# Kernel optimization log

Measured on AMD Instinct MI355X. Metric: run time of the kernel, lower is better.

## Reference

```python
import jax, jax.numpy as jnp
import numpy as np

D_MODEL = 1024
NHEAD = 16
D_K = D_MODEL // NHEAD  # 64
B, L = 2, 2048


def _apply_rotary(x, cos, sin):
    # x: (B, H, L, d_k); cos/sin: (B, L, d_k//2)
    d_half = x.shape[-1] // 2
    x1, x2 = x[..., :d_half], x[..., d_half:]
    c = cos[:, None, :, :]
    s = sin[:, None, :, :]
    return jnp.concatenate([x1 * c - x2 * s, x1 * s + x2 * c], axis=-1)


def setup_inputs() -> dict:
    key = jax.random.key(0)
    ks = jax.random.split(key, 7)
    x = jax.random.normal(ks[0], (B, L, D_MODEL), dtype=jnp.float32)
    rope_cos = jax.random.uniform(ks[1], (B, L, D_K // 2), dtype=jnp.float32)
    rope_sin = jax.random.uniform(ks[2], (B, L, D_K // 2), dtype=jnp.float32)
    # Linear params (PyTorch layout: weight (out, in), y = x @ W.T + b)
    lim_qkv = 1.0 / np.sqrt(D_MODEL)
    W_qkv = jax.random.uniform(ks[3], (3 * D_MODEL, D_MODEL), dtype=jnp.float32, minval=-lim_qkv, maxval=lim_qkv)
    b_qkv = jax.random.uniform(ks[4], (3 * D_MODEL,), dtype=jnp.float32, minval=-lim_qkv, maxval=lim_qkv)
    W_out = jax.random.uniform(ks[5], (D_MODEL, D_MODEL), dtype=jnp.float32, minval=-lim_qkv, maxval=lim_qkv)
    b_out = jax.random.uniform(ks[6], (D_MODEL,), dtype=jnp.float32, minval=-lim_qkv, maxval=lim_qkv)
    return {"x": x, "rope_cos": rope_cos, "rope_sin": rope_sin,
            "W_qkv": W_qkv, "b_qkv": b_qkv, "W_out": W_out, "b_out": b_out}


def reference(x, rope_cos, rope_sin, W_qkv, b_qkv, W_out, b_out):
    Bx, Lx, D = x.shape
    scale = D_K ** -0.5
    qkv = x @ W_qkv.T + b_qkv                     # (B, L, 3D)
    qkv = qkv.reshape(Bx, Lx, 3, NHEAD, D_K)
    q = jnp.transpose(qkv[:, :, 0], (0, 2, 1, 3))  # (B, H, L, d_k)
    k = jnp.transpose(qkv[:, :, 1], (0, 2, 1, 3))
    v = jnp.transpose(qkv[:, :, 2], (0, 2, 1, 3))
    q = _apply_rotary(q, rope_cos, rope_sin)
    k = _apply_rotary(k, rope_cos, rope_sin)
    attn = jnp.einsum("bhqd,bhkd->bhqk", q, k) * scale  # (B, H, L, L)
    attn = jax.nn.softmax(attn, axis=-1)
    out = jnp.einsum("bhqk,bhkd->bhqd", attn, v)          # (B, H, L, d_k)
    out = jnp.transpose(out, (0, 2, 1, 3)).reshape(Bx, Lx, D)
    return out @ W_out.T + b_out
```

## Files before the change

kernel.cpp:

```cpp
#include <hip/hip_runtime.h>
#include <hip/hip_bf16.h>
#include <stdint.h>


typedef __attribute__((ext_vector_type(8)))  short bf16x8;
typedef __attribute__((ext_vector_type(4)))  float f32x4;
typedef __attribute__((ext_vector_type(16))) float f32x16;
typedef __attribute__((ext_vector_type(4)))  short short4v;
typedef __attribute__((ext_vector_type(4)))  unsigned int u32x4;

#define DEV static __device__ __forceinline__

DEV short f2bf(float f) {
  uint32_t u = __builtin_bit_cast(uint32_t, f);
  u += 0x7FFFu + ((u >> 16) & 1u);
  return (short)(u >> 16);
}
DEV float bf2f(short s) {
  return __builtin_bit_cast(float, ((uint32_t)(uint16_t)s) << 16);
}
DEV uint32_t pkbf(float a, float b) {
  __hip_bfloat162 h = __float22bfloat162_rn(make_float2(a, b));
  uint32_t u;
  __builtin_memcpy(&u, &h, 4);
  return u;
}
DEV void pl32swap(uint32_t &dst, uint32_t &src) {
  asm volatile("v_permlane32_swap_b32 %0, %1" : "+v"(dst), "+v"(src));
}

#define AS1 __attribute__((address_space(1)))
#define AS3 __attribute__((address_space(3)))
#define GLOAD_LDS16(gp, lp) \
  __builtin_amdgcn_global_load_lds((const AS1 void*)(gp), (AS3 void*)(lp), 16, 0, 0)

__global__ void k_cvt_all(const float* __restrict__ x, const float* __restrict__ wq,
                          const float* __restrict__ wo,
                          short* __restrict__ xb, short* __restrict__ wqb,
                          short* __restrict__ wob) {
  int bid = blockIdx.x;
  const float* in;
  short* out;
  int i;
  if (bid < 4096)      { in = x;  out = xb;  i = bid * 256 + threadIdx.x; }
  else if (bid < 7168) { in = wq; out = wqb; i = (bid - 4096) * 256 + threadIdx.x; }
  else                 { in = wo; out = wob; i = (bid - 7168) * 256 + threadIdx.x; }
  float4 v = reinterpret_cast<const float4*>(in)[i];
  short4v o = { f2bf(v.x), f2bf(v.y), f2bf(v.z), f2bf(v.w) };
  reinterpret_cast<short4v*>(out)[i] = o;
}

DEV void gemm_stage(const short* Ag, const short* Bg, int K_,
                    short* AsD, short* BsD, int tid) {
  #pragma unroll
  for (int p = 0; p < 4; ++p) {
    int f = p * 256 + tid;
    int row = f >> 3;
    int sch = (f & 7) ^ (row & 7);
    GLOAD_LDS16(Ag + (size_t)row * K_ + sch * 8, AsD + f * 8);
    GLOAD_LDS16(Bg + (size_t)row * K_ + sch * 8, BsD + f * 8);
  }
}

#define GEMM_BODY(A_, Bt_, K_)                                              \
  __shared__ short Lds[4 * 128 * 64];    \
  const int tid = threadIdx.x;                                              \
  const int lane = tid & 63;                                                \
  const int wid  = tid >> 6;                                                \
  const int lq = lane & 15, lg = lane >> 4;                                 \
  const int wr = wid >> 1, wc = wid & 1;                                    \
  int lin_ = blockIdx.y * gridDim.x + blockIdx.x;                           \
  const int q_ = (gridDim.x * gridDim.y) >> 3;                              \
  lin_ = (lin_ & 7) * q_ + (lin_ >> 3);                                     \
  const int m0 = (lin_ / gridDim.x) * 128;                                  \
  const int n0 = (lin_ % gridDim.x) * 128;                                  \
  f32x4 acc[4][4];                                                          \
  _Pragma("unroll")                                                         \
  for (int i = 0; i < 4; ++i)                                               \
    _Pragma("unroll")                                                       \
    for (int j = 0; j < 4; ++j) acc[i][j] = (f32x4){0.f, 0.f, 0.f, 0.f};    \
  const int KT = (K_) >> 6;                                                 \
  gemm_stage((A_) + (size_t)m0 * (K_), (Bt_) + (size_t)n0 * (K_), (K_),     \
             Lds, Lds + 8192, tid);                                         \
  __syncthreads();                                                          \
  int gbuf = 0;                                                             \
  for (int kt = 0; kt < KT; ++kt) {                                         \
    if (kt + 1 < KT)                                                        \
      gemm_stage((A_)  + (size_t)m0 * (K_) + (kt + 1) * 64,                 \
                 (Bt_) + (size_t)n0 * (K_) + (kt + 1) * 64, (K_),           \
                 Lds + (gbuf ^ 1) * 16384,                                  \
                 Lds + (gbuf ^ 1) * 16384 + 8192, tid);                     \
    const short* As = Lds + gbuf * 16384;                                   \
    const short* Bs = As + 8192;                                            \
    _Pragma("unroll")                                                       \
    for (int kk = 0; kk < 2; ++kk) {                                        \
      bf16x8 af[4], bfr[4];                                                 \
      _Pragma("unroll")                                                     \
      for (int i = 0; i < 4; ++i)                                           \
        af[i]  = *reinterpret_cast<const bf16x8*>(                          \
            &As[(wr*64 + i*16 + lq) * 64 + (((kk*4 + lg) ^ (lq & 7)) * 8)]);\
      _Pragma("unroll")                                                     \
      for (int j = 0; j < 4; ++j)                                           \
        bfr[j] = *reinterpret_cast<const bf16x8*>(                          \
            &Bs[(wc*64 + j*16 + lq) * 64 + (((kk*4 + lg) ^ (lq & 7)) * 8)]);\
      _Pragma("unroll")                                                     \
      for (int i = 0; i < 4; ++i)                                           \
        _Pragma("unroll")                                                   \
        for (int j = 0; j < 4; ++j)                                         \
          acc[i][j] = __builtin_amdgcn_mfma_f32_16x16x32_bf16(              \
              af[i], bfr[j], acc[i][j], 0, 0, 0);                           \
    }                                                                       \
    __syncthreads();                                                        \
    gbuf ^= 1;                                                              \
  }

__global__ __launch_bounds__(256) void k_gemm_qkv(
    const short* __restrict__ A, const short* __restrict__ Bt,
    const float* __restrict__ bias,
    const float* __restrict__ cosb, const float* __restrict__ sinb,
    short* __restrict__ Qb, short* __restrict__ Kb, short* __restrict__ Vt)
{
  GEMM_BODY(A, Bt, 1024)

  short* Ep = Lds + wid * 4096;
  const int cglob = n0 + wc * 64;
  if (cglob < 2048) {
    const bool isq = (cglob < 1024);
    const float QS = isq ? 0.125f * 1.4426950408889634f : 1.0f;
    short* dst = isq ? Qb : Kb;
    const int h = (cglob & 1023) >> 6;
    const float b0 = bias[cglob + lq],      b2 = bias[cglob + 32 + lq];
    const float b1 = bias[cglob + 16 + lq], b3 = bias[cglob + 48 + lq];
    #pragma unroll
    for (int i = 0; i < 4; ++i) {
      #pragma unroll
      for (int r = 0; r < 4; ++r) {
        int lloc = i*16 + lg*4 + r;
        int rg = m0 + wr*64 + lloc;
        float c0 = cosb[(size_t)rg * 32 + lq];
        float s0 = sinb[(size_t)rg * 32 + lq];
        float c1 = cosb[(size_t)rg * 32 + 16 + lq];
        float s1 = sinb[(size_t)rg * 32 + 16 + lq];
        float x1 = acc[i][0][r] + b0, x2 = acc[i][2][r] + b2;
        Ep[lloc*64 + lq]      = f2bf((x1 * c0 - x2 * s0) * QS);
        Ep[lloc*64 + 32 + lq] = f2bf((x1 * s0 + x2 * c0) * QS);
        float y1 = acc[i][1][r] + b1, y2 = acc[i][3][r] + b3;
        Ep[lloc*64 + 16 + lq] = f2bf((y1 * c1 - y2 * s1) * QS);
        Ep[lloc*64 + 48 + lq] = f2bf((y1 * s1 + y2 * c1) * QS);
      }
    }
    #pragma unroll
    for (int p = 0; p < 8; ++p) {
      int f = p * 64 + lane;
      int lloc = f >> 3, d0 = (f & 7) * 8;
      int rg = m0 + wr*64 + lloc;
      int bi = rg >> 11, ll = rg & 2047;
      bf16x8 v = *reinterpret_cast<const bf16x8*>(&Ep[lloc*64 + d0]);
      *reinterpret_cast<bf16x8*>(
          &dst[((size_t)(bi * 16 + h) * 2048 + ll) * 64 + d0]) = v;
    }
  } else {
    const int h = (cglob - 2048) >> 6;
    #pragma unroll
    for (int i = 0; i < 4; ++i) {
      int lloc = i*16 + lg*4;
      #pragma unroll
      for (int j = 0; j < 4; ++j) {
        int d = j * 16 + lq;
        float bv = bias[cglob + d];
        short4v pk4 = { f2bf(acc[i][j][0] + bv), f2bf(acc[i][j][1] + bv),
                        f2bf(acc[i][j][2] + bv), f2bf(acc[i][j][3] + bv) };
        *reinterpret_cast<short4v*>(
            &Ep[d*64 + (lloc ^ ((d & 7) << 3))]) = pk4;
      }
    }
    #pragma unroll
    for (int p = 0; p < 8; ++p) {
      int f = p * 64 + lane;
      int d = f >> 3, lc = (f & 7) * 8;
      bf16x8 v = *reinterpret_cast<const bf16x8*>(&Ep[d*64 + lc]);
      int lreal = lc ^ ((d & 7) << 3);
      int rg = m0 + wr*64 + lreal;
      int bi = rg >> 11, ll = rg & 2047;
      *reinterpret_cast<bf16x8*>(
          &Vt[((size_t)(bi * 16 + h) * 64 + d) * 2048 + ll]) = v;
    }
  }
}

__global__ __launch_bounds__(256) void k_gemm_out(
    const short* __restrict__ A, const short* __restrict__ Bt,
    const float* __restrict__ bias, float* __restrict__ C)
{
  GEMM_BODY(A, Bt, 1024)
  const int N = 1024;
  #pragma unroll
  for (int i = 0; i < 4; ++i) {
    int rbase = m0 + wr*64 + i*16 + lg*4;
    #pragma unroll
    for (int j = 0; j < 4; ++j) {
      int col = n0 + wc*64 + j*16 + lq;
      float bv = bias[col];
      #pragma unroll
      for (int r = 0; r < 4; ++r)
        C[(size_t)(rbase + r) * N + col] = acc[i][j][r] + bv;
    }
  }
}

__global__ __launch_bounds__(256, 4) void k_attn(
    const short* __restrict__ Q, const short* __restrict__ Kb,
    const short* __restrict__ Vt,
    short* __restrict__ P0, short* __restrict__ P1,
    float* __restrict__ L0, float* __restrict__ L1)
{
  __shared__ short Ks[2][64 * 64];
  __shared__ short Vs[2][64 * 64];
  const int tid = threadIdx.x;
  const int lane = tid & 63;
  const int wid  = tid >> 6;
  const int Lq = lane & 31;
  const int h  = lane >> 5;
  const int bh = blockIdx.y;
  const int q0 = blockIdx.x * 128 + wid * 32;
  const int b = bh >> 4, hh = bh & 15;
  const int t0 = blockIdx.z * 16;
  short* Pp = blockIdx.z ? P1 : P0;
  float* Lp = blockIdx.z ? L1 : L0;

  const short* Qp = Q  + ((size_t)bh * 2048 + q0 + Lq) * 64;
  const short* Kp = Kb + (size_t)bh * 2048 * 64;
  const short* Vp = Vt + (size_t)bh * 64 * 2048;

  #define STAGE_KV(c, t) do {                                              \
    const short* Kg_ = Kp + (size_t)(t) * 64 * 64;                         \
    const short* Vg_ = Vp + (size_t)(t) * 64;                              \
    _Pragma("unroll")                                                      \
    for (int p_ = 0; p_ < 2; ++p_) {                                       \
      int f_ = p_ * 256 + tid;                                             \
      int row_ = f_ >> 3;                                                  \
      int sch_ = (f_ & 7) ^ (row_ & 7);                                    \
      GLOAD_LDS16(Kg_ + row_ * 64 + sch_ * 8,            &Ks[c][f_ * 8]);  \
      GLOAD_LDS16(Vg_ + (size_t)row_ * 2048 + sch_ * 8,  &Vs[c][f_ * 8]);  \
    }                                                                      \
  } while (0)

  bf16x8 qf[4];
  #pragma unroll
  for (int ks = 0; ks < 4; ++ks)
    qf[ks] = *reinterpret_cast<const bf16x8*>(Qp + ks * 16 + h * 8);

  f32x16 o[2];
  #pragma unroll
  for (int nd = 0; nd < 2; ++nd)
    #pragma unroll
    for (int r = 0; r < 16; ++r) o[nd][r] = 0.f;
  float la0 = 0.f, la1 = 0.f;

  STAGE_KV(0, t0);
  asm volatile("s_waitcnt vmcnt(0)" ::: "memory");
  __syncthreads();

  for (int kk2 = 0; kk2 < 16; ++kk2) {
    const int cur = kk2 & 1;
    if (kk2 < 15) STAGE_KV(cur ^ 1, t0 + kk2 + 1);

    #pragma unroll
    for (int mb = 0; mb < 2; ++mb) {
      f32x16 sm;
      #pragma unroll
      for (int r = 0; r < 16; ++r) sm[r] = 0.f;
      #pragma unroll
      for (int ks = 0; ks < 4; ++ks) {
        bf16x8 kf = *reinterpret_cast<const bf16x8*>(
            &Ks[cur][(mb*32 + Lq) * 64 + (((ks*2 + h) ^ (Lq & 7)) * 8)]);
        sm = __builtin_amdgcn_mfma_f32_32x32x16_bf16(kf, qf[ks], sm, 0, 0, 0);
      }
      #pragma unroll
      for (int half = 0; half < 2; ++half) {
        float e0 = __builtin_amdgcn_exp2f(sm[8*half + 0]);
        float e1 = __builtin_amdgcn_exp2f(sm[8*half + 1]);
        float e2 = __builtin_amdgcn_exp2f(sm[8*half + 2]);
        float e3 = __builtin_amdgcn_exp2f(sm[8*half + 3]);
        float e4 = __builtin_amdgcn_exp2f(sm[8*half + 4]);
        float e5 = __builtin_amdgcn_exp2f(sm[8*half + 5]);
        float e6 = __builtin_amdgcn_exp2f(sm[8*half + 6]);
        float e7 = __builtin_amdgcn_exp2f(sm[8*half + 7]);
        la0 += (e0 + e1) + (e4 + e5);
        la1 += (e2 + e3) + (e6 + e7);
        uint32_t w0 = pkbf(e0, e1), w1 = pkbf(e2, e3);
        uint32_t w2 = pkbf(e4, e5), w3 = pkbf(e6, e7);
        pl32swap(w0, w2);
        pl32swap(w1, w3);
        u32x4 paw = { w0, w1, w2, w3 };
        bf16x8 pa = __builtin_bit_cast(bf16x8, paw);
        const int ksl = mb * 2 + half;
        #pragma unroll
        for (int nd = 0; nd < 2; ++nd) {
          bf16x8 vf = *reinterpret_cast<const bf16x8*>(
              &Vs[cur][(nd*32 + Lq) * 64 + (((ksl*2 + h) ^ (Lq & 7)) * 8)]);
          o[nd] = __builtin_amdgcn_mfma_f32_32x32x16_bf16(pa, vf, o[nd], 0, 0, 0);
        }
      }
    }
    asm volatile("s_waitcnt vmcnt(0)" ::: "memory");
    __syncthreads();
  }

  float l_part = la0 + la1;
  l_part += __shfl_xor(l_part, 32, 64);
  if (h == 0) Lp[((size_t)bh << 11) + q0 + Lq] = l_part;
  #pragma unroll
  for (int r = 0; r < 16; ++r) {
    int qrow = (r & 3) + 8 * (r >> 2) + 4 * h;
    size_t rowb = ((size_t)b * 2048 + q0 + qrow) * 1024 + hh * 64;
    Pp[rowb + Lq]      = f2bf(o[0][r]);
    Pp[rowb + 32 + Lq] = f2bf(o[1][r]);
  }
  #undef STAGE_KV
}

__global__ void k_merge(const short* __restrict__ P0, const short* __restrict__ P1,
                        const float* __restrict__ L0, const float* __restrict__ L1,
                        short* __restrict__ AO)
{
  int idx = blockIdx.x * 256 + threadIdx.x;
  int rg = idx >> 7;
  int c0 = (idx & 127) * 8;
  int bh = ((rg >> 11) << 4) + (c0 >> 6);
  size_t lix = ((size_t)bh << 11) + (rg & 2047);
  float inv = 1.f / (L0[lix] + L1[lix]);
  size_t off = (size_t)rg * 1024 + c0;
  bf16x8 a = *reinterpret_cast<const bf16x8*>(&P0[off]);
  bf16x8 bv = *reinterpret_cast<const bf16x8*>(&P1[off]);
  bf16x8 r;
  #pragma unroll
  for (int j = 0; j < 8; ++j)
    r[j] = f2bf((bf2f(a[j]) + bf2f(bv[j])) * inv);
  *reinterpret_cast<bf16x8*>(&AO[off]) = r;
}

extern "C" void kernel_launch(void* const* d_in, const int* in_sizes, int n_in,
                              void* d_out, int out_size, void* d_ws, size_t ws_size,
                              hipStream_t stream) {
  (void)in_sizes; (void)n_in; (void)out_size; (void)ws_size;
  const float* x    = (const float*)d_in[0];
  const float* rc   = (const float*)d_in[1];
  const float* rs   = (const float*)d_in[2];
  const float* Wqkv = (const float*)d_in[3];
  const float* bqkv = (const float*)d_in[4];
  const float* Wout = (const float*)d_in[5];
  const float* bout = (const float*)d_in[6];
  float* out = (float*)d_out;

  char* ws = (char*)d_ws;
  short* xb  = (short*)(ws);
  short* wqb = (short*)(ws + 8388608);
  short* wob = (short*)(ws + 14680064);
  short* Qb  = (short*)(ws + 16777216);
  short* Kb  = (short*)(ws + 25165824);
  short* Vt  = (short*)(ws + 33554432);
  short* P0  = (short*)(ws + 41943040);
  short* P1  = (short*)(ws + 50331648);
  float* L0  = (float*)(ws + 58720256);
  float* L1  = (float*)(ws + 58982400);

  k_cvt_all<<<8192, 256, 0, stream>>>(x, Wqkv, Wout, xb, wqb, wob);
  k_gemm_qkv<<<dim3(24, 32), 256, 0, stream>>>(xb, wqb, bqkv, rc, rs, Qb, Kb, Vt);
  k_attn<<<dim3(16, 32, 2), 256, 0, stream>>>(Qb, Kb, Vt, P0, P1, L0, L1);
  k_merge<<<2048, 256, 0, stream>>>(P0, P1, L0, L1, P0);
  k_gemm_out<<<dim3(8, 32), 256, 0, stream>>>(P0, wob, bout, out);
}
```

Measured before the change: 115.3 us.

## Use 4-stage LDS pipeline with K=32 slices and vmcnt waits in GEMMs

Replaces the double-buffered 64-wide K tiles with a four-stage ring of 32-wide K slices in the same LDS footprint. Three slices are prefetched ahead, and partial s_waitcnt vmcnt waits with a single barrier per step replace the full __syncthreads pair, so global-to-LDS loads overlap deeper with MFMA work. It changes the XOR swizzle for the narrower rows. The cost is more loop iterations with fewer MFMAs each and hand-tuned wait counts that must match the issued load count.

After: 115.1 us. About the same (-0.2%).

```diff
diff --git a/kernel.cpp b/kernel.cpp
--- a/kernel.cpp
+++ b/kernel.cpp
@@ -50,20 +50,8 @@
   reinterpret_cast<short4v*>(out)[i] = o;
 }
 
-DEV void gemm_stage(const short* Ag, const short* Bg, int K_,
-                    short* AsD, short* BsD, int tid) {
-  #pragma unroll
-  for (int p = 0; p < 4; ++p) {
-    int f = p * 256 + tid;
-    int row = f >> 3;
-    int sch = (f & 7) ^ (row & 7);
-    GLOAD_LDS16(Ag + (size_t)row * K_ + sch * 8, AsD + f * 8);
-    GLOAD_LDS16(Bg + (size_t)row * K_ + sch * 8, BsD + f * 8);
-  }
-}
-
 #define GEMM_BODY(A_, Bt_, K_)                                              \
-  __shared__ short Lds[4 * 128 * 64];    \
+  __shared__ short Lds[4 * 8192];           \
   const int tid = threadIdx.x;                                              \
   const int lane = tid & 63;                                                \
   const int wid  = tid >> 6;                                                \
@@ -79,40 +67,50 @@
   for (int i = 0; i < 4; ++i)                                               \
     _Pragma("unroll")                                                       \
     for (int j = 0; j < 4; ++j) acc[i][j] = (f32x4){0.f, 0.f, 0.f, 0.f};    \
-  const int KT = (K_) >> 6;                                                 \
-  gemm_stage((A_) + (size_t)m0 * (K_), (Bt_) + (size_t)n0 * (K_), (K_),     \
-             Lds, Lds + 8192, tid);                                         \
-  __syncthreads();                                                          \
-  int gbuf = 0;                                                             \
-  for (int kt = 0; kt < KT; ++kt) {                                         \
-    if (kt + 1 < KT)                                                        \
-      gemm_stage((A_)  + (size_t)m0 * (K_) + (kt + 1) * 64,                 \
-                 (Bt_) + (size_t)n0 * (K_) + (kt + 1) * 64, (K_),           \
-                 Lds + (gbuf ^ 1) * 16384,                                  \
-                 Lds + (gbuf ^ 1) * 16384 + 8192, tid);                     \
-    const short* As = Lds + gbuf * 16384;                                   \
-    const short* Bs = As + 8192;                                            \
-    _Pragma("unroll")                                                       \
-    for (int kk = 0; kk < 2; ++kk) {                                        \
-      bf16x8 af[4], bfr[4];                                                 \
-      _Pragma("unroll")                                                     \
-      for (int i = 0; i < 4; ++i)                                           \
-        af[i]  = *reinterpret_cast<const bf16x8*>(                          \
-            &As[(wr*64 + i*16 + lq) * 64 + (((kk*4 + lg) ^ (lq & 7)) * 8)]);\
+  const short* Ag_ = (A_)  + (size_t)m0 * (K_);                             \
+  const short* Bg_ = (Bt_) + (size_t)n0 * (K_);                             \
+  const int HS = (K_) >> 5;                            \
+  auto STG = [&](int s, int t) {                                            \
+    short* base_ = Lds + s * 8192;                                          \
+    _Pragma("unroll")                                                       \
+    for (int p_ = 0; p_ < 2; ++p_) {                                        \
+      int f_ = p_ * 256 + tid;              \
+      int row_ = f_ >> 2;                                                   \
+      int g_ = (f_ & 3) ^ ((f_ >> 3) & 3);                                  \
+      GLOAD_LDS16(Ag_ + (size_t)row_ * (K_) + (t) * 32 + g_ * 8,            \
+                  base_ + f_ * 8);                                          \
+      GLOAD_LDS16(Bg_ + (size_t)row_ * (K_) + (t) * 32 + g_ * 8,            \
+                  base_ + 4096 + f_ * 8);                                   \
+    }                                                                       \
+  };                                                                        \
+  STG(0, 0); STG(1, 1); STG(2, 2);                                          \
+  const int sA_ = (lq >> 1) & 3;        \
+  for (int hh = 0; hh < HS; ++hh) {                                         \
+    if (hh < HS - 2)       asm volatile("s_waitcnt vmcnt(8)" ::: "memory"); \
+    else if (hh == HS - 2) asm volatile("s_waitcnt vmcnt(4)" ::: "memory"); \
+    else                   asm volatile("s_waitcnt vmcnt(0)" ::: "memory"); \
+    __builtin_amdgcn_s_barrier();                                           \
+    asm volatile("" ::: "memory");                                          \
+    if (hh + 3 < HS) STG((hh + 3) & 3, hh + 3);                             \
+    const short* As = Lds + (hh & 3) * 8192;                                \
+    const short* Bs = As + 4096;                                            \
+    bf16x8 af[4], bfr[4];                                                   \
+    _Pragma("unroll")                                                       \
+    for (int i = 0; i < 4; ++i)                                             \
+      af[i]  = *reinterpret_cast<const bf16x8*>(                            \
+          &As[(wr*64 + i*16 + lq) * 32 + ((lg ^ sA_) * 8)]);                \
+    _Pragma("unroll")                                                       \
+    for (int j = 0; j < 4; ++j)                                             \
+      bfr[j] = *reinterpret_cast<const bf16x8*>(                            \
+          &Bs[(wc*64 + j*16 + lq) * 32 + ((lg ^ sA_) * 8)]);                \
+    _Pragma("unroll")                                                       \
+    for (int i = 0; i < 4; ++i)                                             \
       _Pragma("unroll")                                                     \
       for (int j = 0; j < 4; ++j)                                           \
-        bfr[j] = *reinterpret_cast<const bf16x8*>(                          \
-            &Bs[(wc*64 + j*16 + lq) * 64 + (((kk*4 + lg) ^ (lq & 7)) * 8)]);\
-      _Pragma("unroll")                                                     \
-      for (int i = 0; i < 4; ++i)                                           \
-        _Pragma("unroll")                                                   \
-        for (int j = 0; j < 4; ++j)                                         \
-          acc[i][j] = __builtin_amdgcn_mfma_f32_16x16x32_bf16(              \
-              af[i], bfr[j], acc[i][j], 0, 0, 0);                           \
-    }                                                                       \
-    __syncthreads();                                                        \
-    gbuf ^= 1;                                                              \
-  }
+        acc[i][j] = __builtin_amdgcn_mfma_f32_16x16x32_bf16(                \
+            af[i], bfr[j], acc[i][j], 0, 0, 0);                             \
+  }                                                                         \
+  __syncthreads();
 
 __global__ __launch_bounds__(256) void k_gemm_qkv(
     const short* __restrict__ A, const short* __restrict__ Bt,
```
